# Performance work log

Measured on AMD Instinct MI355X. Metric: run time of the kernel, lower is better.

Reference implementation:

```python
import jax, jax.numpy as jnp
import numpy as np

B, CIN, COUT, H, W, K, G = 2, 256, 256, 128, 128, 3, 4
PAD = (K - 1) // 2


def setup_inputs() -> dict:
    key = jax.random.key(0)
    k1, k2, k3, k4 = jax.random.split(key, 4)
    x = jax.random.normal(k1, (B, CIN, H, W), dtype=jnp.float32)
    # conv_offset: 1x1 conv, out channels = G*2*K*K. (Zero-init in the module; use
    # small random weights so offsets are non-trivial for correctness testing.)
    w_offset = jax.random.normal(k2, (G * 2 * K * K, CIN), dtype=jnp.float32) * 0.01
    b_offset = jax.random.normal(k3, (G * 2 * K * K,), dtype=jnp.float32) * 0.5
    # DeformConv weight (bias=False in mmcv DeformConv)
    w_deform = jax.random.normal(k4, (COUT, CIN, K, K), dtype=jnp.float32) * (1.0 / np.sqrt(CIN * K * K))
    return {"x": x, "w_offset": w_offset, "b_offset": b_offset, "w_deform": w_deform}


def _bilinear_gather(img, y, x):
    """img: [B,G,Cg,H,W]; y,x: [B,G,H,W] float sample coords -> [B,G,Cg,H,W].
    Zero padding outside the image (mmcv DCN bilinear semantics)."""
    b, g, cg, h, w = img.shape
    imgf = img.reshape(b, g, cg, h * w)
    y0 = jnp.floor(y)
    x0 = jnp.floor(x)
    out = jnp.zeros((b, g, cg, h * w), img.dtype)
    for yy, xx in ((y0, x0), (y0, x0 + 1.0), (y0 + 1.0, x0), (y0 + 1.0, x0 + 1.0)):
        wgt = (1.0 - jnp.abs(y - yy)) * (1.0 - jnp.abs(x - xx))
        valid = (yy >= 0) & (yy < h) & (xx >= 0) & (xx < w)
        wgt = jnp.where(valid, wgt, 0.0)
        yi = jnp.clip(yy, 0, h - 1).astype(jnp.int32)
        xi = jnp.clip(xx, 0, w - 1).astype(jnp.int32)
        idx = (yi * w + xi).reshape(b, g, 1, h * w)
        vals = jnp.take_along_axis(imgf, jnp.broadcast_to(idx, (b, g, cg, h * w)), axis=3)
        out = out + wgt.reshape(b, g, 1, h * w) * vals
    return out.reshape(b, g, cg, h, w)


def reference(x, w_offset, b_offset, w_deform):
    b, cin, h, w = x.shape
    cout, _, k, _ = w_deform.shape
    pad = (k - 1) // 2
    # 1x1 offset conv
    offset = jnp.einsum('bchw,oc->bohw', x, w_offset) + b_offset[None, :, None, None]
    g = offset.shape[1] // (2 * k * k)
    off = offset.reshape(b, g, k * k, 2, h, w)  # (dy, dx) per kernel tap, mmcv layout
    xg = x.reshape(b, g, cin // g, h, w)
    hh = jnp.arange(h, dtype=x.dtype)[:, None]
    ww = jnp.arange(w, dtype=x.dtype)[None, :]
    out = jnp.zeros((b, cout, h, w), x.dtype)
    for i in range(k):
        for j in range(k):
            t = i * k + j
            ys = hh - pad + i + off[:, :, t, 0]  # [B,G,H,W]
            xs = ww - pad + j + off[:, :, t, 1]
            samp = _bilinear_gather(xg, ys, xs).reshape(b, cin, h, w)
            out = out + jnp.einsum('bchw,oc->bohw', samp, w_deform[:, :, i, j])
    return jax.nn.relu(out)
```

## Files before the change

kernel.cpp:

```cpp
#include <hip/hip_runtime.h>
#include <stdint.h>

#define HW    16384
#define CIN   256
#define COUT  256
#define Hh    128
#define Ww    128
#define OFFC  72

typedef __attribute__((ext_vector_type(4))) float    f32x4;
typedef __attribute__((ext_vector_type(2))) _Float16 f16x2;
typedef __attribute__((ext_vector_type(8))) _Float16 f16x8;
typedef unsigned short u16;
typedef unsigned int   u32;

__device__ __forceinline__ u16 f2h(float f) { return __builtin_bit_cast(u16, (_Float16)f); }
__device__ __forceinline__ u32 pk2(float f) { u32 h = f2h(f); return h | (h << 16); }
__device__ __forceinline__ f16x2 bch(u32 u) { return __builtin_bit_cast(f16x2, u); }

__global__ __launch_bounds__(256) void kprep(const float* __restrict__ x, const float* __restrict__ wd,
                                             const float* __restrict__ wo, u16* __restrict__ xt,
                                             u16* __restrict__ wfrag, u16* __restrict__ wfrag2) {
  __shared__ float smem[8 * 576];
  int blk = blockIdx.x;
  if (blk < 2048) {
    int bg = blk >> 8;
    int p0 = (blk & 255) << 6;
    int pq = threadIdx.x & 15;
    int cs = threadIdx.x >> 4;
    const float* src = x + (size_t)bg * 64 * HW + p0 + pq * 4;
    u32* lds = (u32*)smem;
    #pragma unroll
    for (int s = 0; s < 2; ++s) {
      int c2 = cs + 16 * s;
      f32x4 lo = *(const f32x4*)(src + (size_t)(2 * c2 + 0) * HW);
      f32x4 hi = *(const f32x4*)(src + (size_t)(2 * c2 + 1) * HW);
      #pragma unroll
      for (int j = 0; j < 4; ++j) {
        int px = pq * 4 + j;
        u32 pkv = (u32)f2h(lo[j]) | ((u32)f2h(hi[j]) << 16);
        lds[px * 36 + ((c2 + px) & 31)] = pkv;
      }
    }
    __syncthreads();
    u16* dstb = xt + ((size_t)bg * HW + p0) * 64;
    #pragma unroll
    for (int r = 0; r < 2; ++r) {
      int e  = r * 256 + threadIdx.x;
      int px = e >> 3, c4 = e & 7;
      u32 w[4];
      #pragma unroll
      for (int m = 0; m < 4; ++m)
        w[m] = lds[px * 36 + ((4 * c4 + m + px) & 31)];
      *(uint4*)(dstb + (size_t)e * 8) = make_uint4(w[0], w[1], w[2], w[3]);
    }
  } else if (blk < 2176) {
    int bb = blk - 2048;
    int nh = bb & 31;
    int g  = bb >> 5;
    const float* src = wd + (size_t)(nh * 8) * 2304 + (size_t)g * 64 * 9;
    #pragma unroll
    for (int r = 0; r < 18; ++r) {
      int idx = threadIdx.x + 256 * r;
      int cl  = idx / 576;
      int rem = idx - cl * 576;
      smem[cl * 576 + rem] = src[(size_t)cl * 2304 + rem];
    }
    __syncthreads();
    int nt = nh >> 1, nb = (nh & 1) * 8;
    #pragma unroll
    for (int r = 0; r < 18; ++r) {
      int o  = threadIdx.x + 256 * r;
      int j  = o & 7;
      int n8 = (o >> 3) & 7;
      int q  = (o >> 6) & 3;
      int kcl = o >> 8;
      int t = kcl >> 1, half = kcl & 1;
      int cg = half * 32 + q * 8 + j;
      float v = smem[n8 * 576 + cg * 9 + t];
      int kc = (g * 9 + t) * 2 + half;
      int lane = q * 16 + nb + n8;
      wfrag[((size_t)(kc * 16 + nt) * 64 + lane) * 8 + j] = f2h(v);
    }
  } else {
    int e = (blk - 2176) * 256 + threadIdx.x;
    int j = e & 7;
    int lane = (e >> 3) & 63;
    int idx = e >> 9;
    int kc = idx / 5, nt = idx - 5 * kc;
    int n16 = lane & 15, q = lane >> 4;
    int oc = nt * 16 + n16;
    int c  = kc * 32 + q * 8 + j;
    float v = (oc < OFFC) ? wo[(size_t)oc * CIN + c] : 0.f;
    wfrag2[e] = f2h(v);
  }
}

__device__ __forceinline__ void mkpre(float yy, float xx, int* ob, u32* wp) {
  float y0f = floorf(yy), x0f = floorf(xx);
  float fy = yy - y0f, fx = xx - x0f;
  int y0 = (int)y0f, x0 = (int)x0f;
  int y1 = y0 + 1, x1 = x0 + 1;
  float vy0 = (y0 >= 0 && y0 < Hh) ? 1.f : 0.f;
  float vy1 = (y1 >= 0 && y1 < Hh) ? 1.f : 0.f;
  float vx0 = (x0 >= 0 && x0 < Ww) ? 1.f : 0.f;
  float vx1 = (x1 >= 0 && x1 < Ww) ? 1.f : 0.f;
  wp[0] = pk2((1.f - fy) * (1.f - fx) * vy0 * vx0);
  wp[1] = pk2((1.f - fy) * fx * vy0 * vx1);
  wp[2] = pk2(fy * (1.f - fx) * vy1 * vx0);
  wp[3] = pk2(fy * fx * vy1 * vx1);
  int cy0 = min(max(y0, 0), Hh - 1), cy1 = min(max(y1, 0), Hh - 1);
  int cx0 = min(max(x0, 0), Ww - 1), cx1 = min(max(x1, 0), Ww - 1);
  ob[0] = (cy0 * Ww + cx0) << 7;
  ob[1] = (cy0 * Ww + cx1) << 7;
  ob[2] = (cy1 * Ww + cx0) << 7;
  ob[3] = (cy1 * Ww + cx1) << 7;
}

__device__ __forceinline__ uint4 bil16(const uint4* v, const u32* wp) {
  f16x2 W0 = bch(wp[0]), W1 = bch(wp[1]), W2 = bch(wp[2]), W3 = bch(wp[3]);
  uint4 r;
  { f16x2 s = bch(v[0].x) * W0 + bch(v[1].x) * W1 + bch(v[2].x) * W2 + bch(v[3].x) * W3; r.x = __builtin_bit_cast(u32, s); }
  { f16x2 s = bch(v[0].y) * W0 + bch(v[1].y) * W1 + bch(v[2].y) * W2 + bch(v[3].y) * W3; r.y = __builtin_bit_cast(u32, s); }
  { f16x2 s = bch(v[0].z) * W0 + bch(v[1].z) * W1 + bch(v[2].z) * W2 + bch(v[3].z) * W3; r.z = __builtin_bit_cast(u32, s); }
  { f16x2 s = bch(v[0].w) * W0 + bch(v[1].w) * W1 + bch(v[2].w) * W2 + bch(v[3].w) * W3; r.w = __builtin_bit_cast(u32, s); }
  return r;
}

__global__ __launch_bounds__(1024, 4) void k2(const u16* __restrict__ xt, const u16* __restrict__ wfrag2,
                                              const float* __restrict__ bo, const u16* __restrict__ wfrag,
                                              float* __restrict__ out) {
  __shared__ u16   astage[2 * 16 * 512];
  __shared__ float offl[128 * 74];
  int tid  = threadIdx.x;
  int lane = tid & 63, n16 = lane & 15, q = (tid >> 4) & 3;
  int wv   = tid >> 6;
  int sp   = wv >> 1;
  int hp   = wv & 1;
  int blk  = blockIdx.x;
  int swz  = (blk & 7) * 32 + (blk >> 3);
  int b  = swz >> 7;
  int p0 = (swz & 127) << 7;
  int h  = p0 >> 7;
  const char* xtb = (const char*)xt + (size_t)b * 4 * HW * 128;
  float fh  = (float)h;
  float fxp = (float)(sp * 16 + n16);
  int   chb = hp * 64 + q * 16;
  int   pxl = sp * 16 + n16;

  f32x4 acc[8];
  #pragma unroll
  for (int mt = 0; mt < 8; ++mt) acc[mt] = (f32x4){0.f, 0.f, 0.f, 0.f};

  if (wv < 8) {
    f32x4 oacc[5];
    #pragma unroll
    for (int nt = 0; nt < 5; ++nt) {
      int oc = nt * 16 + n16;
      float bv = (oc < OFFC) ? bo[oc] : 0.f;
      oacc[nt] = (f32x4){bv, bv, bv, bv};
    }
    #pragma unroll
    for (int kc = 0; kc < 8; ++kc) {
      int g = kc >> 1;
      f16x8 af = __builtin_bit_cast(f16x8, *(const uint4*)(xtb +
          ((size_t)(g * HW + p0 + wv * 16 + n16)) * 128 + (kc & 1) * 64 + q * 16));
      #pragma unroll
      for (int nt = 0; nt < 5; ++nt) {
        f16x8 bfo = __builtin_bit_cast(f16x8, *(const uint4*)(wfrag2 + (size_t)(((kc * 5 + nt) << 6) + lane) * 8));
        oacc[nt] = __builtin_amdgcn_mfma_f32_16x16x32_f16(af, bfo, oacc[nt], 0, 0, 0);
      }
    }
    #pragma unroll
    for (int nt = 0; nt < 5; ++nt) {
      int oc = nt * 16 + n16;
      if (oc < OFFC) {
        #pragma unroll
        for (int r = 0; r < 4; ++r)
          offl[(wv * 16 + q * 4 + r) * 74 + oc] = oacc[nt][r];
      }
    }
  }

  uint4 dA[4], dB[4];
  u32   wpA[4], wpB[4];
  uint4 bfA[2], bfB[2];

  auto bfld = [&](int gt, uint4* bf) {
    const u16* wb = wfrag + ((size_t)((2 * gt) * 16 + wv) * 64 + lane) * 8;
    bf[0] = *(const uint4*)(wb);
    bf[1] = *(const uint4*)(wb + 8192);
  };

  bfld(0, bfA);
  __syncthreads();

  auto issue = [&](int gt, uint4* dd, u32* wpp) {
    float oy = offl[pxl * 74 + gt * 2];
    float ox = offl[pxl * 74 + gt * 2 + 1];
    int g = (gt * 57) >> 9;
    int t = gt - g * 9;
    int i = (t * 683) >> 11;
    int j = t - i * 3;
    int ob[4];
    mkpre(fh + (float)(i - 1) + oy, fxp + (float)(j - 1) + ox, ob, wpp);
    const char* xg = xtb + (size_t)g * HW * 128;
    #pragma unroll
    for (int c = 0; c < 4; ++c)
      dd[c] = *(const uint4*)(xg + ob[c] + chb);
  };
  auto consume = [&](int slot, uint4* bf) {
    #pragma unroll
    for (int mt = 0; mt < 8; ++mt) {
      f16x8 af0 = __builtin_bit_cast(f16x8,
          *(const uint4*)&astage[(slot * 16 + mt * 2 + 0) * 512 + lane * 8]);
      acc[mt] = __builtin_amdgcn_mfma_f32_16x16x32_f16(af0, __builtin_bit_cast(f16x8, bf[0]), acc[mt], 0, 0, 0);
      f16x8 af1 = __builtin_bit_cast(f16x8,
          *(const uint4*)&astage[(slot * 16 + mt * 2 + 1) * 512 + lane * 8]);
      acc[mt] = __builtin_amdgcn_mfma_f32_16x16x32_f16(af1, __builtin_bit_cast(f16x8, bf[1]), acc[mt], 0, 0, 0);
    }
  };

  issue(0, dA, wpA);
  issue(1, dB, wpB);
  *(uint4*)&astage[(0 * 16 + sp * 2 + hp) * 512 + lane * 8] = bil16(dA, wpA);
  __syncthreads();

  #pragma unroll 1
  for (int gt = 0; gt < 36; gt += 2) {
    *(uint4*)&astage[(1 * 16 + sp * 2 + hp) * 512 + lane * 8] = bil16(dB, wpB);
    bfld(gt + 1, bfB);
    if (gt + 2 < 36) issue(gt + 2, dA, wpA);
    consume(0, bfA);
    __syncthreads();
    if (gt + 2 < 36) {
      *(uint4*)&astage[(0 * 16 + sp * 2 + hp) * 512 + lane * 8] = bil16(dA, wpA);
      bfld(gt + 2, bfA);
      issue(gt + 3, dB, wpB);
    }
    consume(1, bfB);
    __syncthreads();
  }

  float* op = out + (size_t)b * COUT * HW + p0;
  int cout = wv * 16 + n16;
  #pragma unroll
  for (int mt = 0; mt < 8; ++mt) {
    f32x4 v = acc[mt];
    #pragma unroll
    for (int r = 0; r < 4; ++r) v[r] = fmaxf(v[r], 0.f);
    *(f32x4*)(op + (size_t)cout * HW + mt * 16 + q * 4) = v;
  }
}

extern "C" void kernel_launch(void* const* d_in, const int* in_sizes, int n_in,
                              void* d_out, int out_size, void* d_ws, size_t ws_size,
                              hipStream_t stream) {
  const float* x  = (const float*)d_in[0];
  const float* wo = (const float*)d_in[1];
  const float* bo = (const float*)d_in[2];
  const float* wd = (const float*)d_in[3];
  float* out = (float*)d_out;

  u16* xtp    = (u16*)d_ws;
  u16* wfrag  = (u16*)((char*)d_ws + 16777216);
  u16* wfrag2 = (u16*)((char*)d_ws + 16777216 + 1179648);

  kprep<<<2256, 256, 0, stream>>>(x, wd, wo, xtp, wfrag, wfrag2);
  k2   <<<256, 1024, 0, stream>>>(xtp, wfrag2, bo, wfrag, out);
}
```

Measured before the change: 176.0 us.

## Specialize waves into gather producers and MFMA consumers

Splits the 16 waves of each block into 8 producer waves and 8 consumer waves. Producers compute offsets and bilinear samples into double-buffered LDS. Consumers run the MFMA GEMM, each covering 32 output channels with doubled accumulators. The aim is to overlap gather latency with matrix math instead of having every wave alternate between both. It doubles per-wave gather work on producers and register use on consumers, which may cause spills or make the gather side the bottleneck.

```diff
diff --git a/kernel.cpp b/kernel.cpp
--- a/kernel.cpp
+++ b/kernel.cpp
@@ -135,8 +135,6 @@
   int tid  = threadIdx.x;
   int lane = tid & 63, n16 = lane & 15, q = (tid >> 4) & 3;
   int wv   = tid >> 6;
-  int sp   = wv >> 1;
-  int hp   = wv & 1;
   int blk  = blockIdx.x;
   int swz  = (blk & 7) * 32 + (blk >> 3);
   int b  = swz >> 7;
@@ -144,112 +142,139 @@
   int h  = p0 >> 7;
   const char* xtb = (const char*)xt + (size_t)b * 4 * HW * 128;
   float fh  = (float)h;
-  float fxp = (float)(sp * 16 + n16);
-  int   chb = hp * 64 + q * 16;
-  int   pxl = sp * 16 + n16;
-
-  f32x4 acc[8];
-  #pragma unroll
-  for (int mt = 0; mt < 8; ++mt) acc[mt] = (f32x4){0.f, 0.f, 0.f, 0.f};
 
   if (wv < 8) {
-    f32x4 oacc[5];
-    #pragma unroll
-    for (int nt = 0; nt < 5; ++nt) {
-      int oc = nt * 16 + n16;
-      float bv = (oc < OFFC) ? bo[oc] : 0.f;
-      oacc[nt] = (f32x4){bv, bv, bv, bv};
-    }
-    #pragma unroll
-    for (int kc = 0; kc < 8; ++kc) {
-      int g = kc >> 1;
-      f16x8 af = __builtin_bit_cast(f16x8, *(const uint4*)(xtb +
-          ((size_t)(g * HW + p0 + wv * 16 + n16)) * 128 + (kc & 1) * 64 + q * 16));
+    int sp = wv;
+    float fxp = (float)(sp * 16 + n16);
+    int   pxl = sp * 16 + n16;
+
+    {
+      f32x4 oacc[5];
       #pragma unroll
       for (int nt = 0; nt < 5; ++nt) {
-        f16x8 bfo = __builtin_bit_cast(f16x8, *(const uint4*)(wfrag2 + (size_t)(((kc * 5 + nt) << 6) + lane) * 8));
-        oacc[nt] = __builtin_amdgcn_mfma_f32_16x16x32_f16(af, bfo, oacc[nt], 0, 0, 0);
-      }
-    }
-    #pragma unroll
-    for (int nt = 0; nt < 5; ++nt) {
-      int oc = nt * 16 + n16;
-      if (oc < OFFC) {
+        int oc = nt * 16 + n16;
+        float bv = (oc < OFFC) ? bo[oc] : 0.f;
+        oacc[nt] = (f32x4){bv, bv, bv, bv};
+      }
+      #pragma unroll
+      for (int kc = 0; kc < 8; ++kc) {
+        int g = kc >> 1;
+        f16x8 af = __builtin_bit_cast(f16x8, *(const uint4*)(xtb +
+            ((size_t)(g * HW + p0 + sp * 16 + n16)) * 128 + (kc & 1) * 64 + q * 16));
         #pragma unroll
-        for (int r = 0; r < 4; ++r)
-          offl[(wv * 16 + q * 4 + r) * 74 + oc] = oacc[nt][r];
-      }
-    }
-  }
-
-  uint4 dA[4], dB[4];
-  u32   wpA[4], wpB[4];
-  uint4 bfA[2], bfB[2];
-
-  auto bfld = [&](int gt, uint4* bf) {
-    const u16* wb = wfrag + ((size_t)((2 * gt) * 16 + wv) * 64 + lane) * 8;
-    bf[0] = *(const uint4*)(wb);
-    bf[1] = *(const uint4*)(wb + 8192);
-  };
-
-  bfld(0, bfA);
-  __syncthreads();
-
-  auto issue = [&](int gt, uint4* dd, u32* wpp) {
-    float oy = offl[pxl * 74 + gt * 2];
-    float ox = offl[pxl * 74 + gt * 2 + 1];
-    int g = (gt * 57) >> 9;
-    int t = gt - g * 9;
-    int i = (t * 683) >> 11;
-    int j = t - i * 3;
-    int ob[4];
-    mkpre(fh + (float)(i - 1) + oy, fxp + (float)(j - 1) + ox, ob, wpp);
-    const char* xg = xtb + (size_t)g * HW * 128;
-    #pragma unroll
-    for (int c = 0; c < 4; ++c)
-      dd[c] = *(const uint4*)(xg + ob[c] + chb);
-  };
-  auto consume = [&](int slot, uint4* bf) {
+        for (int nt = 0; nt < 5; ++nt) {
+          f16x8 bfo = __builtin_bit_cast(f16x8, *(const uint4*)(wfrag2 + (size_t)(((kc * 5 + nt) << 6) + lane) * 8));
+          oacc[nt] = __builtin_amdgcn_mfma_f32_16x16x32_f16(af, bfo, oacc[nt], 0, 0, 0);
+        }
+      }
+      #pragma unroll
+      for (int nt = 0; nt < 5; ++nt) {
+        int oc = nt * 16 + n16;
+        if (oc < OFFC) {
+          #pragma unroll
+          for (int r = 0; r < 4; ++r)
+            offl[(sp * 16 + q * 4 + r) * 74 + oc] = oacc[nt][r];
+        }
+      }
+    }
+    __syncthreads();
+
+    uint4 dA0[4], dA1[4], dB0[4], dB1[4];
+    u32   wpA[4], wpB[4];
+
+    auto issue = [&](int gt, uint4* d0, uint4* d1, u32* wpp) {
+      float oy = offl[pxl * 74 + gt * 2];
+      float ox = offl[pxl * 74 + gt * 2 + 1];
+      int g = (gt * 57) >> 9;
+      int t = gt - g * 9;
+      int i = (t * 683) >> 11;
+      int j = t - i * 3;
+      int ob[4];
+      mkpre(fh + (float)(i - 1) + oy, fxp + (float)(j - 1) + ox, ob, wpp);
+      const char* xg = xtb + (size_t)g * HW * 128 + q * 16;
+      #pragma unroll
+      for (int c = 0; c < 4; ++c) {
+        d0[c] = *(const uint4*)(xg + ob[c]);
+        d1[c] = *(const uint4*)(xg + ob[c] + 64);
+      }
+    };
+    auto stage = [&](int buf, uint4* d0, uint4* d1, u32* wpp) {
+      *(uint4*)&astage[(buf * 16 + sp * 2 + 0) * 512 + lane * 8] = bil16(d0, wpp);
+      *(uint4*)&astage[(buf * 16 + sp * 2 + 1) * 512 + lane * 8] = bil16(d1, wpp);
+    };
+
+    issue(0, dA0, dA1, wpA);
+    issue(1, dB0, dB1, wpB);
+    stage(0, dA0, dA1, wpA);
+    __syncthreads();
+
+    #pragma unroll 1
+    for (int gt = 0; gt < 36; gt += 2) {
+      stage(1, dB0, dB1, wpB);
+      if (gt + 2 < 36) issue(gt + 2, dA0, dA1, wpA);
+      __syncthreads();
+      if (gt + 2 < 36) {
+        stage(0, dA0, dA1, wpA);
+        issue(gt + 3, dB0, dB1, wpB);
+      }
+      __syncthreads();
+    }
+  } else {
+    int cv = wv - 8;
+
+    f32x4 acc[8][2];
     #pragma unroll
     for (int mt = 0; mt < 8; ++mt) {
-      f16x8 af0 = __builtin_bit_cast(f16x8,
-          *(const uint4*)&astage[(slot * 16 + mt * 2 + 0) * 512 + lane * 8]);
-      acc[mt] = __builtin_amdgcn_mfma_f32_16x16x32_f16(af0, __builtin_bit_cast(f16x8, bf[0]), acc[mt], 0, 0, 0);
-      f16x8 af1 = __builtin_bit_cast(f16x8,
-          *(const uint4*)&astage[(slot * 16 + mt * 2 + 1) * 512 + lane * 8]);
-      acc[mt] = __builtin_amdgcn_mfma_f32_16x16x32_f16(af1, __builtin_bit_cast(f16x8, bf[1]), acc[mt], 0, 0, 0);
-    }
-  };
-
-  issue(0, dA, wpA);
-  issue(1, dB, wpB);
-  *(uint4*)&astage[(0 * 16 + sp * 2 + hp) * 512 + lane * 8] = bil16(dA, wpA);
-  __syncthreads();
-
-  #pragma unroll 1
-  for (int gt = 0; gt < 36; gt += 2) {
-    *(uint4*)&astage[(1 * 16 + sp * 2 + hp) * 512 + lane * 8] = bil16(dB, wpB);
-    bfld(gt + 1, bfB);
-    if (gt + 2 < 36) issue(gt + 2, dA, wpA);
-    consume(0, bfA);
-    __syncthreads();
-    if (gt + 2 < 36) {
-      *(uint4*)&astage[(0 * 16 + sp * 2 + hp) * 512 + lane * 8] = bil16(dA, wpA);
-      bfld(gt + 2, bfA);
-      issue(gt + 3, dB, wpB);
-    }
-    consume(1, bfB);
-    __syncthreads();
-  }
-
-  float* op = out + (size_t)b * COUT * HW + p0;
-  int cout = wv * 16 + n16;
-  #pragma unroll
-  for (int mt = 0; mt < 8; ++mt) {
-    f32x4 v = acc[mt];
-    #pragma unroll
-    for (int r = 0; r < 4; ++r) v[r] = fmaxf(v[r], 0.f);
-    *(f32x4*)(op + (size_t)cout * HW + mt * 16 + q * 4) = v;
+      acc[mt][0] = (f32x4){0.f, 0.f, 0.f, 0.f};
+      acc[mt][1] = (f32x4){0.f, 0.f, 0.f, 0.f};
+    }
+    uint4 bfA[4], bfB[4];
+    auto bfld = [&](int gt, uint4* bf) {
+      const u16* wb = wfrag + ((size_t)((2 * gt) * 16 + 2 * cv) * 64 + lane) * 8;
+      bf[0] = *(const uint4*)(wb);
+      bf[1] = *(const uint4*)(wb + 512);
+      bf[2] = *(const uint4*)(wb + 8192);
+      bf[3] = *(const uint4*)(wb + 8704);
+    };
+    auto consume = [&](int slot, uint4* bf) {
+      #pragma unroll
+      for (int mt = 0; mt < 8; ++mt) {
+        f16x8 af0 = __builtin_bit_cast(f16x8,
+            *(const uint4*)&astage[(slot * 16 + mt * 2 + 0) * 512 + lane * 8]);
+        acc[mt][0] = __builtin_amdgcn_mfma_f32_16x16x32_f16(af0, __builtin_bit_cast(f16x8, bf[0]), acc[mt][0], 0, 0, 0);
+        acc[mt][1] = __builtin_amdgcn_mfma_f32_16x16x32_f16(af0, __builtin_bit_cast(f16x8, bf[1]), acc[mt][1], 0, 0, 0);
+        f16x8 af1 = __builtin_bit_cast(f16x8,
+            *(const uint4*)&astage[(slot * 16 + mt * 2 + 1) * 512 + lane * 8]);
+        acc[mt][0] = __builtin_amdgcn_mfma_f32_16x16x32_f16(af1, __builtin_bit_cast(f16x8, bf[2]), acc[mt][0], 0, 0, 0);
+        acc[mt][1] = __builtin_amdgcn_mfma_f32_16x16x32_f16(af1, __builtin_bit_cast(f16x8, bf[3]), acc[mt][1], 0, 0, 0);
+      }
+    };
+
+    bfld(0, bfA);
+    __syncthreads();
+    __syncthreads();
+
+    #pragma unroll 1
+    for (int gt = 0; gt < 36; gt += 2) {
+      bfld(gt + 1, bfB);
+      consume(0, bfA);
+      __syncthreads();
+      if (gt + 2 < 36) bfld(gt + 2, bfA);
+      consume(1, bfB);
+      __syncthreads();
+    }
+
+    float* op = out + (size_t)b * COUT * HW + p0;
+    #pragma unroll
+    for (int mt = 0; mt < 8; ++mt)
+      #pragma unroll
+      for (int j = 0; j < 2; ++j) {
+        f32x4 v = acc[mt][j];
+        #pragma unroll
+        for (int r = 0; r < 4; ++r) v[r] = fmaxf(v[r], 0.f);
+        int cout = cv * 32 + j * 16 + n16;
+        *(f32x4*)(op + (size_t)cout * HW + mt * 16 + q * 4) = v;
+      }
   }
 }
 
```

Result: slower. 183.0 us (+4.0%).

## Deepen gather pipeline to three LDS stages, recompute bilinear weights at stage time

Applied to the files above, without the earlier changes.

Moves the gather/MFMA software pipeline from a double-buffered A stage to a triple-buffered one, so bilinear gathers are issued three taps ahead of use rather than two. The bilinear weights are now recomputed from the offsets when the data is staged, instead of being kept in registers from issue time. This frees registers to hold the extra in-flight gather data. The aim is to hide more global gather latency behind the MFMA work. In exchange the kernel uses more LDS and repeats the floor/offset arithmetic, which may affect occupancy at 1024-thread blocks.

```diff
diff --git a/kernel.cpp b/kernel.cpp
--- a/kernel.cpp
+++ b/kernel.cpp
@@ -96,7 +96,18 @@
   }
 }
 
-__device__ __forceinline__ void mkpre(float yy, float xx, int* ob, u32* wp) {
+__device__ __forceinline__ void mkaddr(float yy, float xx, int* ob) {
+  float y0f = floorf(yy), x0f = floorf(xx);
+  int y0 = (int)y0f, x0 = (int)x0f;
+  int y1 = y0 + 1, x1 = x0 + 1;
+  int cy0 = min(max(y0, 0), Hh - 1), cy1 = min(max(y1, 0), Hh - 1);
+  int cx0 = min(max(x0, 0), Ww - 1), cx1 = min(max(x1, 0), Ww - 1);
+  ob[0] = (cy0 * Ww + cx0) << 7;
+  ob[1] = (cy0 * Ww + cx1) << 7;
+  ob[2] = (cy1 * Ww + cx0) << 7;
+  ob[3] = (cy1 * Ww + cx1) << 7;
+}
+__device__ __forceinline__ void mkwgt(float yy, float xx, u32* wp) {
   float y0f = floorf(yy), x0f = floorf(xx);
   float fy = yy - y0f, fx = xx - x0f;
   int y0 = (int)y0f, x0 = (int)x0f;
@@ -109,12 +120,6 @@
   wp[1] = pk2((1.f - fy) * fx * vy0 * vx1);
   wp[2] = pk2(fy * (1.f - fx) * vy1 * vx0);
   wp[3] = pk2(fy * fx * vy1 * vx1);
-  int cy0 = min(max(y0, 0), Hh - 1), cy1 = min(max(y1, 0), Hh - 1);
-  int cx0 = min(max(x0, 0), Ww - 1), cx1 = min(max(x1, 0), Ww - 1);
-  ob[0] = (cy0 * Ww + cx0) << 7;
-  ob[1] = (cy0 * Ww + cx1) << 7;
-  ob[2] = (cy1 * Ww + cx0) << 7;
-  ob[3] = (cy1 * Ww + cx1) << 7;
 }
 
 __device__ __forceinline__ uint4 bil16(const uint4* v, const u32* wp) {
@@ -130,7 +135,7 @@
 __global__ __launch_bounds__(1024, 4) void k2(const u16* __restrict__ xt, const u16* __restrict__ wfrag2,
                                               const float* __restrict__ bo, const u16* __restrict__ wfrag,
                                               float* __restrict__ out) {
-  __shared__ u16   astage[2 * 16 * 512];
+  __shared__ u16   astage[3 * 16 * 512];
   __shared__ float offl[128 * 74];
   int tid  = threadIdx.x;
   int lane = tid & 63, n16 = lane & 15, q = (tid >> 4) & 3;
@@ -182,20 +187,15 @@
     }
   }
 
-  uint4 dA[4], dB[4];
-  u32   wpA[4], wpB[4];
-  uint4 bfA[2], bfB[2];
+  uint4 SA[4], SB[4], SC[4];
+  uint4 bfA[2], bfB[2], bfC[2];
 
   auto bfld = [&](int gt, uint4* bf) {
     const u16* wb = wfrag + ((size_t)((2 * gt) * 16 + wv) * 64 + lane) * 8;
     bf[0] = *(const uint4*)(wb);
     bf[1] = *(const uint4*)(wb + 8192);
   };
-
-  bfld(0, bfA);
-  __syncthreads();
-
-  auto issue = [&](int gt, uint4* dd, u32* wpp) {
+  auto issue = [&](int gt, uint4* dd) {
     float oy = offl[pxl * 74 + gt * 2];
     float ox = offl[pxl * 74 + gt * 2 + 1];
     int g = (gt * 57) >> 9;
@@ -203,11 +203,22 @@
     int i = (t * 683) >> 11;
     int j = t - i * 3;
     int ob[4];
-    mkpre(fh + (float)(i - 1) + oy, fxp + (float)(j - 1) + ox, ob, wpp);
+    mkaddr(fh + (float)(i - 1) + oy, fxp + (float)(j - 1) + ox, ob);
     const char* xg = xtb + (size_t)g * HW * 128;
     #pragma unroll
     for (int c = 0; c < 4; ++c)
       dd[c] = *(const uint4*)(xg + ob[c] + chb);
+  };
+  auto stage = [&](int slot, int gt, uint4* dd) {
+    float oy = offl[pxl * 74 + gt * 2];
+    float ox = offl[pxl * 74 + gt * 2 + 1];
+    int g = (gt * 57) >> 9;
+    int t = gt - g * 9;
+    int i = (t * 683) >> 11;
+    int j = t - i * 3;
+    u32 wp[4];
+    mkwgt(fh + (float)(i - 1) + oy, fxp + (float)(j - 1) + ox, wp);
+    *(uint4*)&astage[(slot * 16 + sp * 2 + hp) * 512 + lane * 8] = bil16(dd, wp);
   };
   auto consume = [&](int slot, uint4* bf) {
     #pragma unroll
@@ -221,24 +232,34 @@
     }
   };
 
-  issue(0, dA, wpA);
-  issue(1, dB, wpB);
-  *(uint4*)&astage[(0 * 16 + sp * 2 + hp) * 512 + lane * 8] = bil16(dA, wpA);
+  bfld(0, bfA);
   __syncthreads();
 
+  issue(0, SA);
+  issue(1, SB);
+  issue(2, SC);
+  stage(0, 0, SA);
+  issue(3, SA);
+  __syncthreads();
+
   #pragma unroll 1
-  for (int gt = 0; gt < 36; gt += 2) {
-    *(uint4*)&astage[(1 * 16 + sp * 2 + hp) * 512 + lane * 8] = bil16(dB, wpB);
+  for (int gt = 0; gt < 36; gt += 3) {
+    stage(1, gt + 1, SB);
     bfld(gt + 1, bfB);
-    if (gt + 2 < 36) issue(gt + 2, dA, wpA);
+    if (gt + 4 < 36) issue(gt + 4, SB);
     consume(0, bfA);
     __syncthreads();
-    if (gt + 2 < 36) {
-      *(uint4*)&astage[(0 * 16 + sp * 2 + hp) * 512 + lane * 8] = bil16(dA, wpA);
-      bfld(gt + 2, bfA);
-      issue(gt + 3, dB, wpB);
-    }
+    stage(2, gt + 2, SC);
+    bfld(gt + 2, bfC);
+    if (gt + 5 < 36) issue(gt + 5, SC);
     consume(1, bfB);
+    __syncthreads();
+    if (gt + 3 < 36) {
+      stage(0, gt + 3, SA);
+      bfld(gt + 3, bfA);
+    }
+    if (gt + 6 < 36) issue(gt + 6, SA);
+    consume(2, bfC);
     __syncthreads();
   }
 
```

New measurement: 192.5 us. 1.09x slower.

## Retile GEMM warps into 2x4 pixel-by-cout blocks to cut LDS A-fragment reads

Applied to the files above, without the earlier changes.

Each of the 16 waves previously computed 16 output channels across all 128 pixels, reading every A fragment from LDS once per wave. Waves now own a 32-pixel by 64-channel tile, loading 4 B fragments per k-step from global memory and reusing each LDS A fragment across 4 MFMAs. This cuts LDS read traffic per MFMA. In exchange it raises global weight loads per wave and drops the one-step-ahead prefetch of weight fragments, so those loads now sit on the critical path just before the MFMAs.

```diff
diff --git a/kernel.cpp b/kernel.cpp
--- a/kernel.cpp
+++ b/kernel.cpp
@@ -137,6 +137,8 @@
   int wv   = tid >> 6;
   int sp   = wv >> 1;
   int hp   = wv & 1;
+  int P    = wv & 3;
+  int C    = wv >> 2;
   int blk  = blockIdx.x;
   int swz  = (blk & 7) * 32 + (blk >> 3);
   int b  = swz >> 7;
@@ -148,9 +150,11 @@
   int   chb = hp * 64 + q * 16;
   int   pxl = sp * 16 + n16;
 
-  f32x4 acc[8];
+  f32x4 acc[2][4];
   #pragma unroll
-  for (int mt = 0; mt < 8; ++mt) acc[mt] = (f32x4){0.f, 0.f, 0.f, 0.f};
+  for (int m = 0; m < 2; ++m)
+    #pragma unroll
+    for (int i = 0; i < 4; ++i) acc[m][i] = (f32x4){0.f, 0.f, 0.f, 0.f};
 
   if (wv < 8) {
     f32x4 oacc[5];
@@ -181,19 +185,10 @@
       }
     }
   }
+  __syncthreads();
 
   uint4 dA[4], dB[4];
   u32   wpA[4], wpB[4];
-  uint4 bfA[2], bfB[2];
-
-  auto bfld = [&](int gt, uint4* bf) {
-    const u16* wb = wfrag + ((size_t)((2 * gt) * 16 + wv) * 64 + lane) * 8;
-    bf[0] = *(const uint4*)(wb);
-    bf[1] = *(const uint4*)(wb + 8192);
-  };
-
-  bfld(0, bfA);
-  __syncthreads();
 
   auto issue = [&](int gt, uint4* dd, u32* wpp) {
     float oy = offl[pxl * 74 + gt * 2];
@@ -209,15 +204,26 @@
     for (int c = 0; c < 4; ++c)
       dd[c] = *(const uint4*)(xg + ob[c] + chb);
   };
-  auto consume = [&](int slot, uint4* bf) {
-    #pragma unroll
-    for (int mt = 0; mt < 8; ++mt) {
+  auto consume = [&](int slot, int gt) {
+    const u16* wb = wfrag + ((size_t)((2 * gt) * 16 + 4 * C) * 64 + lane) * 8;
+    uint4 bf0[4], bf1[4];
+    #pragma unroll
+    for (int i = 0; i < 4; ++i) {
+      bf0[i] = *(const uint4*)(wb + i * 512);
+      bf1[i] = *(const uint4*)(wb + 8192 + i * 512);
+    }
+    #pragma unroll
+    for (int m = 0; m < 2; ++m) {
       f16x8 af0 = __builtin_bit_cast(f16x8,
-          *(const uint4*)&astage[(slot * 16 + mt * 2 + 0) * 512 + lane * 8]);
-      acc[mt] = __builtin_amdgcn_mfma_f32_16x16x32_f16(af0, __builtin_bit_cast(f16x8, bf[0]), acc[mt], 0, 0, 0);
+          *(const uint4*)&astage[(slot * 16 + (2 * P + m) * 2 + 0) * 512 + lane * 8]);
+      #pragma unroll
+      for (int i = 0; i < 4; ++i)
+        acc[m][i] = __builtin_amdgcn_mfma_f32_16x16x32_f16(af0, __builtin_bit_cast(f16x8, bf0[i]), acc[m][i], 0, 0, 0);
       f16x8 af1 = __builtin_bit_cast(f16x8,
-          *(const uint4*)&astage[(slot * 16 + mt * 2 + 1) * 512 + lane * 8]);
-      acc[mt] = __builtin_amdgcn_mfma_f32_16x16x32_f16(af1, __builtin_bit_cast(f16x8, bf[1]), acc[mt], 0, 0, 0);
+          *(const uint4*)&astage[(slot * 16 + (2 * P + m) * 2 + 1) * 512 + lane * 8]);
+      #pragma unroll
+      for (int i = 0; i < 4; ++i)
+        acc[m][i] = __builtin_amdgcn_mfma_f32_16x16x32_f16(af1, __builtin_bit_cast(f16x8, bf1[i]), acc[m][i], 0, 0, 0);
     }
   };
 
@@ -229,28 +235,28 @@
   #pragma unroll 1
   for (int gt = 0; gt < 36; gt += 2) {
     *(uint4*)&astage[(1 * 16 + sp * 2 + hp) * 512 + lane * 8] = bil16(dB, wpB);
-    bfld(gt + 1, bfB);
     if (gt + 2 < 36) issue(gt + 2, dA, wpA);
-    consume(0, bfA);
+    consume(0, gt);
     __syncthreads();
     if (gt + 2 < 36) {
       *(uint4*)&astage[(0 * 16 + sp * 2 + hp) * 512 + lane * 8] = bil16(dA, wpA);
-      bfld(gt + 2, bfA);
       issue(gt + 3, dB, wpB);
     }
-    consume(1, bfB);
+    consume(1, gt + 1);
     __syncthreads();
   }
 
-  float* op = out + (size_t)b * COUT * HW + p0;
-  int cout = wv * 16 + n16;
+  float* op = out + (size_t)b * COUT * HW + p0 + P * 32;
   #pragma unroll
-  for (int mt = 0; mt < 8; ++mt) {
-    f32x4 v = acc[mt];
-    #pragma unroll
-    for (int r = 0; r < 4; ++r) v[r] = fmaxf(v[r], 0.f);
-    *(f32x4*)(op + (size_t)cout * HW + mt * 16 + q * 4) = v;
-  }
+  for (int m = 0; m < 2; ++m)
+    #pragma unroll
+    for (int i = 0; i < 4; ++i) {
+      f32x4 v = acc[m][i];
+      #pragma unroll
+      for (int r = 0; r < 4; ++r) v[r] = fmaxf(v[r], 0.f);
+      int cout = C * 64 + i * 16 + n16;
+      *(f32x4*)(op + (size_t)cout * HW + m * 16 + q * 4) = v;
+    }
 }
 
 extern "C" void kernel_launch(void* const* d_in, const int* in_sizes, int n_in,
```

Result: slower. 204.2 us (+16.0%).
